# Kernel optimization log

Hardware: AMD Instinct MI355X
Metric: run time of the kernel (lower is better)

## Reference

```python
import jax, jax.numpy as jnp
import numpy as np

N_NODES = 100000
N_EDGES = 1600000
IN_DIM = 128
HID_DIM = 128
OUT_DIM = 16
N_GRAPHS = 128


def setup_inputs() -> dict:
    key = jax.random.key(0)
    ks = jax.random.split(key, 8)
    x = jax.random.normal(ks[0], (N_NODES, IN_DIM), dtype=jnp.float32)
    edge_index = jax.random.randint(ks[1], (2, N_EDGES), 0, N_NODES, dtype=jnp.int64)
    batch = jnp.sort(jax.random.randint(ks[2], (N_NODES,), 0, N_GRAPHS, dtype=jnp.int64))
    # GCNConv params (glorot-ish scale) and Linear params
    w1 = jax.random.normal(ks[3], (IN_DIM, HID_DIM), dtype=jnp.float32) / np.sqrt(IN_DIM)
    b1 = jnp.zeros((HID_DIM,), dtype=jnp.float32)
    w2 = jax.random.normal(ks[4], (HID_DIM, HID_DIM), dtype=jnp.float32) / np.sqrt(HID_DIM)
    b2 = jnp.zeros((HID_DIM,), dtype=jnp.float32)
    wc = jax.random.normal(ks[5], (HID_DIM, OUT_DIM), dtype=jnp.float32) / np.sqrt(HID_DIM)
    bc = jnp.zeros((OUT_DIM,), dtype=jnp.float32)
    return {"x": x, "edge_index": edge_index, "batch": batch,
            "w1": w1, "b1": b1, "w2": w2, "b2": b2, "wc": wc, "bc": bc}


def _gcn_layer(h, src, dst, w, b, n_nodes):
    # h: [N, Fin]; src/dst: [E+N] (self-loops already appended)
    h = h @ w  # [N, Fout]
    ones = jnp.ones_like(dst, dtype=h.dtype)
    deg = jax.ops.segment_sum(ones, dst, num_segments=n_nodes)  # [N]
    dinv = jnp.where(deg > 0, jax.lax.rsqrt(deg), 0.0)
    norm = dinv[src] * dinv[dst]  # [E+N]
    msg = h[src] * norm[:, None]  # gather + scale, [E+N, Fout]
    out = jax.ops.segment_sum(msg, dst, num_segments=n_nodes)  # scatter-add
    return out + b


def reference(x, edge_index, batch, w1, b1, w2, b2, wc, bc):
    n = x.shape[0]
    loop = jnp.arange(n, dtype=edge_index.dtype)
    src = jnp.concatenate([edge_index[0], loop])  # add self-loops (PyG default)
    dst = jnp.concatenate([edge_index[1], loop])

    h = jax.nn.relu(_gcn_layer(x, src, dst, w1, b1, n))
    h = jax.nn.relu(_gcn_layer(h, src, dst, w2, b2, n))

    # global mean pool over graphs
    sums = jax.ops.segment_sum(h, batch, num_segments=N_GRAPHS)  # [G, H]
    cnt = jax.ops.segment_sum(jnp.ones((n,), h.dtype), batch, num_segments=N_GRAPHS)
    pooled = sums / jnp.maximum(cnt, 1.0)[:, None]

    return pooled @ wc + bc  # [G, OUT_DIM]
```

## Files before the change

### kernel.cpp

```cpp
#include <hip/hip_runtime.h>
#include <hip/hip_bf16.h>
#include <stdint.h>

#define NN 100000
#define NE 1600000
#define FDIM 128
#define NGRAPH 128
#define ODIM 16
#define NBKT 391
#define CAP 4608
#define PCAP 8704
#define SCHUNK 4096
#define NSCAT ((NE + SCHUNK - 1) / SCHUNK)
#define NSTARTB ((NN + 255) / 256)

typedef __attribute__((ext_vector_type(8))) short short8;
typedef __attribute__((ext_vector_type(8))) unsigned short ushort8;
typedef __attribute__((ext_vector_type(4))) float f32x4;
typedef __attribute__((ext_vector_type(2))) float f32x2;
typedef __attribute__((ext_vector_type(4))) int i32x4;

__device__ __forceinline__ float blo(unsigned int p) { return __uint_as_float(p << 16); }
__device__ __forceinline__ float bhi(unsigned int p) { return __uint_as_float(p & 0xffff0000u); }
__device__ __forceinline__ unsigned short f2b(float f) {
    unsigned int u = __float_as_uint(f);
    unsigned int r = (u + 0x7fffu + ((u >> 16) & 1u)) >> 16;
    return (unsigned short)r;
}
__device__ __forceinline__ unsigned int cvt2(float lo, float hi) {
    __hip_bfloat162 b = __float22bfloat162_rn(float2{lo, hi});
    return *reinterpret_cast<unsigned int*>(&b);
}

__device__ __forceinline__ int detect_w(const int* __restrict__ ei) {
    int lane = threadIdx.x & 63;
    int v = ei[2 * lane + 1];
    return (__ballot(v != 0) == 0ULL) ? 1 : 0;
}
__device__ __forceinline__ int ld_idx(const int* __restrict__ p, long long i, int w) {
    return w ? p[2 * i] : p[i];
}

__global__ void __launch_bounds__(256) k_prep(
    const float* __restrict__ w1, const float* __restrict__ w2,
    unsigned short* __restrict__ wt1, unsigned short* __restrict__ wt2,
    const int* __restrict__ ei, const int* __restrict__ batch,
    int* __restrict__ gstart, int* __restrict__ bcursor,
    unsigned short* __restrict__ xws)
{
    int b = blockIdx.x, t = threadIdx.x;
    if (b < 128) {
        int idx = b * 256 + t;
        int which = idx >> 14, r = idx & 16383;
        int k = r >> 7, j = r & 127;
        const float* w = which ? w2 : w1;
        unsigned short* wt = which ? wt2 : wt1;
        wt[j * 128 + k] = f2b(w[k * 128 + j]);
    } else if (b < 128 + NSTARTB) {
        int w = detect_w(ei);
        int i = (b - 128) * 256 + t;
        if (i < NN) {
            int bb = ld_idx(batch, i, w);
            int prev = (i == 0) ? -1 : ld_idx(batch, i - 1, w);
            for (int g = prev + 1; g <= bb; ++g) gstart[g] = i;
            if (i == NN - 1)
                for (int g = bb + 1; g <= NGRAPH; ++g) gstart[g] = NN;
        }
    } else {
        int i = (b - 128 - NSTARTB) * 256 + t;
        if (i < NBKT) bcursor[i] = i * CAP;
        if (b == 128 + NSTARTB && t < FDIM) xws[(size_t)NN * FDIM + t] = 0;
    }
}

__global__ void __launch_bounds__(512) k_scat(const int* __restrict__ ei,
                                              int* __restrict__ bcursor,
                                              unsigned int* __restrict__ rec) {
    __shared__ int hist[NBKT];
    __shared__ int gbase[NBKT];
    __shared__ int lcur[NBKT];
    int t = threadIdx.x;
    int w = detect_w(ei);
    for (int i = t; i < NBKT; i += 512) hist[i] = 0;
    __syncthreads();
    long long e0 = (long long)blockIdx.x * SCHUNK;
    unsigned int myrec[8];
    int mybkt[8];
    #pragma unroll
    for (int j = 0; j < 8; ++j) {
        long long e = e0 + j * 512 + t;
        if (e < NE) {
            int s = ld_idx(ei, e, w);
            int d = ld_idx(ei, NE + e, w);
            mybkt[j] = d >> 8;
            myrec[j] = (unsigned int)s | ((unsigned int)(d & 255) << 17);
            atomicAdd(&hist[mybkt[j]], 1);
        } else mybkt[j] = -1;
    }
    __syncthreads();
    for (int i = t; i < NBKT; i += 512) {
        int c = hist[i];
        gbase[i] = c ? atomicAdd(&bcursor[i], c) : 0;
        lcur[i] = 0;
    }
    __syncthreads();
    #pragma unroll
    for (int j = 0; j < 8; ++j) {
        int b = mybkt[j];
        if (b >= 0) {
            int r = atomicAdd(&lcur[b], 1);
            int p = gbase[b] + r;
            if (p < (b + 1) * CAP) rec[p] = myrec[j];
        }
    }
}

__global__ void __launch_bounds__(256) k_bucket(const unsigned int* __restrict__ rec,
                                                const int* __restrict__ bcursor,
                                                int* __restrict__ csr,
                                                int2* __restrict__ odeg,
                                                float* __restrict__ dinv) {
    __shared__ unsigned int rbuf[CAP];
    __shared__ int srcout[PCAP];
    __shared__ int hist[256], scn[256], cur[256];
    int b = blockIdx.x, t = threadIdx.x;
    int rbase = b * CAP;
    int cnt = bcursor[b] - rbase;
    if (cnt > CAP) cnt = CAP;
    hist[t] = 0;
    __syncthreads();
    for (int j = t; j < cnt; j += 256) {
        unsigned int r = __builtin_nontemporal_load(&rec[rbase + j]);
        rbuf[j] = r;
        atomicAdd(&hist[r >> 17], 1);
    }
    for (int j = t; j < PCAP; j += 256) srcout[j] = NN << 8;
    __syncthreads();
    int node = (b << 8) + t;
    int v = hist[t];
    int pv = (node < NN) ? ((v + 16) & ~15) : 0;
    scn[t] = pv;
    __syncthreads();
    for (int o = 1; o < 256; o <<= 1) {
        int tv = (t >= o) ? scn[t - o] : 0;
        __syncthreads();
        scn[t] += tv;
        __syncthreads();
    }
    int pexcl = scn[t] - pv;
    cur[t] = pexcl;
    int obase = b * PCAP;
    if (node < NN) {
        odeg[node] = make_int2(obase + pexcl, pv);
        dinv[node] = rsqrtf((float)(v + 1));
        srcout[pexcl + v] = node << 8;
    }
    __syncthreads();
    for (int j = t; j < cnt; j += 256) {
        unsigned int r = rbuf[j];
        int p = atomicAdd(&cur[r >> 17], 1);
        srcout[p] = (int)(r & 0x1FFFFu) << 8;
    }
    __syncthreads();
    int total = scn[255];
    for (int j = t; j < total; j += 256) csr[obase + j] = srcout[j];
}

#define LWS 136
template <bool BF16IN>
__global__ void __launch_bounds__(256) k_gemm(
    const void* __restrict__ Xv,
    const unsigned short* __restrict__ WT,
    const float* __restrict__ dinv,
    unsigned short* __restrict__ OUT)
{
    __shared__ unsigned short lw[128 * LWS];
    int tid = threadIdx.x;
    for (int it = 0; it < 8; ++it) {
        int vidx = it * 256 + tid;
        int j = vidx >> 4, kc = vidx & 15;
        ushort8 v = *(const ushort8*)(WT + j * 128 + kc * 8);
        *(ushort8*)(&lw[j * LWS + kc * 8]) = v;
    }
    __syncthreads();

    int wave = tid >> 6, lane = tid & 63;
    int quad = lane >> 4, n16 = lane & 15;
    int row0 = (blockIdx.x * 4 + wave) * 16;
    if (row0 >= NN) return;

    f32x4 acc[8];
    for (int ct = 0; ct < 8; ++ct) acc[ct] = (f32x4){0.f, 0.f, 0.f, 0.f};

    const int arow = row0 + n16;
    for (int kk = 0; kk < 4; ++kk) {
        short8 a;
        if (BF16IN) {
            a = *(const short8*)((const unsigned short*)Xv + (size_t)arow * 128 + kk * 32 + quad * 8);
        } else {
            const float* ap = (const float*)Xv + (size_t)arow * 128 + kk * 32 + quad * 8;
            float4 a01 = *(const float4*)(ap);
            float4 a23 = *(const float4*)(ap + 4);
            uint4 P;
            P.x = cvt2(a01.x, a01.y);
            P.y = cvt2(a01.z, a01.w);
            P.z = cvt2(a23.x, a23.y);
            P.w = cvt2(a23.z, a23.w);
            a = *(short8*)&P;
        }
        for (int ct = 0; ct < 8; ++ct) {
            short8 b = *(const short8*)(&lw[(ct * 16 + n16) * LWS + kk * 32 + quad * 8]);
            acc[ct] = __builtin_amdgcn_mfma_f32_16x16x32_bf16(a, b, acc[ct], 0, 0, 0);
        }
    }
    for (int r = 0; r < 4; ++r) {
        int row = row0 + quad * 4 + r;
        float dv = dinv[row];
        for (int ct = 0; ct < 8; ++ct)
            OUT[(size_t)row * 128 + ct * 16 + n16] = f2b(acc[ct][r] * dv);
    }
}

__device__ __forceinline__ void acc8(f32x2* a2, uint4 q) {
    a2[0] += (f32x2){blo(q.x), bhi(q.x)};
    a2[1] += (f32x2){blo(q.y), bhi(q.y)};
    a2[2] += (f32x2){blo(q.z), bhi(q.z)};
    a2[3] += (f32x2){blo(q.w), bhi(q.w)};
}

__global__ void __launch_bounds__(256) k_agg(
    const unsigned short* __restrict__ XWS,
    const int* __restrict__ csr,
    const int2* __restrict__ odeg,
    const float* __restrict__ dinv,
    const float* __restrict__ bias,
    unsigned short* __restrict__ H)
{
    int wave = threadIdx.x >> 6, lane = threadIdx.x & 63;
    int v = blockIdx.x * 4 + wave;
    int g = lane >> 4, f = lane & 15;
    int2 od = odeg[v];
    int beg = od.x, pdeg = od.y;
    const char* xb = (const char*)XWS;
    unsigned fo = (unsigned)(f * 16);
    const int* cp = csr + beg + 4 * g;

    f32x2 a2[4];
    a2[0] = (f32x2){0.f, 0.f}; a2[1] = (f32x2){0.f, 0.f};
    a2[2] = (f32x2){0.f, 0.f}; a2[3] = (f32x2){0.f, 0.f};

    int j = 0;
    int pd2 = pdeg & ~31;
    for (; j < pd2; j += 32) {
        i32x4 ca = __builtin_nontemporal_load((const i32x4*)(cp + j));
        i32x4 cb = __builtin_nontemporal_load((const i32x4*)(cp + j + 16));
        uint4 q0 = *(const uint4*)(xb + ((unsigned)ca.x + fo));
        uint4 q1 = *(const uint4*)(xb + ((unsigned)ca.y + fo));
        uint4 q2 = *(const uint4*)(xb + ((unsigned)ca.z + fo));
        uint4 q3 = *(const uint4*)(xb + ((unsigned)ca.w + fo));
        uint4 q4 = *(const uint4*)(xb + ((unsigned)cb.x + fo));
        uint4 q5 = *(const uint4*)(xb + ((unsigned)cb.y + fo));
        uint4 q6 = *(const uint4*)(xb + ((unsigned)cb.z + fo));
        uint4 q7 = *(const uint4*)(xb + ((unsigned)cb.w + fo));
        acc8(a2, q0); acc8(a2, q1); acc8(a2, q2); acc8(a2, q3);
        acc8(a2, q4); acc8(a2, q5); acc8(a2, q6); acc8(a2, q7);
    }
    if (j < pdeg) {
        i32x4 ca = __builtin_nontemporal_load((const i32x4*)(cp + j));
        uint4 q0 = *(const uint4*)(xb + ((unsigned)ca.x + fo));
        uint4 q1 = *(const uint4*)(xb + ((unsigned)ca.y + fo));
        uint4 q2 = *(const uint4*)(xb + ((unsigned)ca.z + fo));
        uint4 q3 = *(const uint4*)(xb + ((unsigned)ca.w + fo));
        acc8(a2, q0); acc8(a2, q1); acc8(a2, q2); acc8(a2, q3);
    }
    #pragma unroll
    for (int i = 0; i < 4; ++i) {
        a2[i].x += __shfl_xor(a2[i].x, 16);
        a2[i].y += __shfl_xor(a2[i].y, 16);
        a2[i].x += __shfl_xor(a2[i].x, 32);
        a2[i].y += __shfl_xor(a2[i].y, 32);
    }
    if (g == 0) {
        float dv = dinv[v];
        float4 b0 = *(const float4*)(bias + f * 8);
        float4 b1 = *(const float4*)(bias + f * 8 + 4);
        uint4 o;
        o.x = cvt2(fmaxf(fmaf(a2[0].x, dv, b0.x), 0.f), fmaxf(fmaf(a2[0].y, dv, b0.y), 0.f));
        o.y = cvt2(fmaxf(fmaf(a2[1].x, dv, b0.z), 0.f), fmaxf(fmaf(a2[1].y, dv, b0.w), 0.f));
        o.z = cvt2(fmaxf(fmaf(a2[2].x, dv, b1.x), 0.f), fmaxf(fmaf(a2[2].y, dv, b1.y), 0.f));
        o.w = cvt2(fmaxf(fmaf(a2[3].x, dv, b1.z), 0.f), fmaxf(fmaf(a2[3].y, dv, b1.w), 0.f));
        *(uint4*)(H + (size_t)v * FDIM + f * 8) = o;
    }
}

__global__ void __launch_bounds__(512) k_poolcls(
    const unsigned short* __restrict__ H, const int* __restrict__ gstart,
    const float* __restrict__ wc, const float* __restrict__ bc,
    float* __restrict__ out)
{
    __shared__ float red[1024];
    __shared__ float pl[FDIM];
    int g = blockIdx.x;
    int t = threadIdx.x;
    int pair = t & 63;
    int seg = t >> 6;
    int beg = gstart[g], end = gstart[g + 1];
    float a0 = 0.f, a1 = 0.f;
    for (int i = beg + seg; i < end; i += 8) {
        unsigned int q = *(const unsigned int*)(H + (size_t)i * FDIM + 2 * pair);
        a0 += blo(q); a1 += bhi(q);
    }
    red[t] = a0; red[512 + t] = a1;
    __syncthreads();
    if (seg == 0) {
        float s0 = 0.f, s1 = 0.f;
        #pragma unroll
        for (int k = 0; k < 8; ++k) {
            s0 += red[pair + 64 * k];
            s1 += red[512 + pair + 64 * k];
        }
        float inv = 1.f / fmaxf((float)(end - beg), 1.f);
        pl[2 * pair] = s0 * inv;
        pl[2 * pair + 1] = s1 * inv;
    }
    __syncthreads();
    if (t < 256) {
        int o = t & 15, fs = t >> 4;
        float acc = 0.f;
        #pragma unroll
        for (int k = 0; k < 8; ++k)
            acc += pl[fs * 8 + k] * wc[(fs * 8 + k) * ODIM + o];
        red[t] = acc;
    }
    __syncthreads();
    if (t < 16) {
        float s = bc[t];
        #pragma unroll
        for (int k = 0; k < 16; ++k) s += red[k * 16 + t];
        out[g * ODIM + t] = s;
    }
}

extern "C" void kernel_launch(void* const* d_in, const int* in_sizes, int n_in,
                              void* d_out, int out_size, void* d_ws, size_t ws_size,
                              hipStream_t stream) {
    const float* x   = (const float*)d_in[0];
    const int* ei    = (const int*)d_in[1];
    const int* batch = (const int*)d_in[2];
    const float* w1  = (const float*)d_in[3];
    const float* b1  = (const float*)d_in[4];
    const float* w2  = (const float*)d_in[5];
    const float* b2  = (const float*)d_in[6];
    const float* wc  = (const float*)d_in[7];
    const float* bc  = (const float*)d_in[8];
    float* out = (float*)d_out;

    char* ws = (char*)d_ws;
    size_t off = 0;
    auto alloc = [&](size_t bytes) -> void* {
        off = (off + 255) & ~(size_t)255;
        void* p = ws + off;
        off += bytes;
        return p;
    };
    int*   bcursor = (int*)alloc(NBKT * 4);
    int2*  odeg    = (int2*)alloc((size_t)NN * 8);
    float* dinv    = (float*)alloc(NN * 4);
    int*   gstart  = (int*)alloc((NGRAPH + 1) * 4);
    unsigned int* rec = (unsigned int*)alloc((size_t)NBKT * CAP * 4);
    int*   csr     = (int*)alloc((size_t)NBKT * PCAP * 4 + 256);
    unsigned short* wt1 = (unsigned short*)alloc(128 * 128 * 2);
    unsigned short* wt2 = (unsigned short*)alloc(128 * 128 * 2);
    unsigned short* xws = (unsigned short*)alloc((size_t)(NN + 1) * FDIM * 2);
    unsigned short* h   = (unsigned short*)alloc((size_t)NN * FDIM * 2);

    k_prep<<<128 + NSTARTB + 2, 256, 0, stream>>>(w1, w2, wt1, wt2, ei, batch, gstart, bcursor, xws);
    k_scat<<<NSCAT, 512, 0, stream>>>(ei, bcursor, rec);
    k_bucket<<<NBKT, 256, 0, stream>>>(rec, bcursor, csr, odeg, dinv);

    k_gemm<false><<<(NN / 16 + 3) / 4, 256, 0, stream>>>(x, wt1, dinv, xws);
    k_agg<<<NN / 4, 256, 0, stream>>>(xws, csr, odeg, dinv, b1, h);
    k_gemm<true><<<(NN / 16 + 3) / 4, 256, 0, stream>>>(h, wt2, dinv, xws);
    k_agg<<<NN / 4, 256, 0, stream>>>(xws, csr, odeg, dinv, b2, h);
    k_poolcls<<<NGRAPH, 512, 0, stream>>>(h, gstart, wc, bc, out);
}
```

Before: 312.8 us.

## Slice feature matrices into 16-column planes for cache-local gather aggregation

Stores the intermediate node-feature matrices as eight 16-feature slices (32 bytes per node per slice) instead of row-major 128-wide rows. Aggregation blocks are now assigned one slice each, and each node is handled by two lanes that read the CSR indices serially. Because a slice covers about 3.2 MB, the random gathers should stay within L2 rather than spanning the full 25 MB feature matrix. The cost is that CSR indices are re-read eight times, per-lane index loads are scalar and serial, and load balance across high-degree nodes gets worse.

```diff
diff --git a/kernel.cpp b/kernel.cpp
--- a/kernel.cpp
+++ b/kernel.cpp
@@ -13,12 +13,13 @@
 #define SCHUNK 4096
 #define NSCAT ((NE + SCHUNK - 1) / SCHUNK)
 #define NSTARTB ((NN + 255) / 256)
+#define SSTR ((NN + 1) * 16)
+#define NAGGB ((((NN) + 127) / 128) * 8)
 
 typedef __attribute__((ext_vector_type(8))) short short8;
 typedef __attribute__((ext_vector_type(8))) unsigned short ushort8;
 typedef __attribute__((ext_vector_type(4))) float f32x4;
 typedef __attribute__((ext_vector_type(2))) float f32x2;
-typedef __attribute__((ext_vector_type(4))) int i32x4;
 
 __device__ __forceinline__ float blo(unsigned int p) { return __uint_as_float(p << 16); }
 __device__ __forceinline__ float bhi(unsigned int p) { return __uint_as_float(p & 0xffff0000u); }
@@ -69,7 +70,10 @@
     } else {
         int i = (b - 128 - NSTARTB) * 256 + t;
         if (i < NBKT) bcursor[i] = i * CAP;
-        if (b == 128 + NSTARTB && t < FDIM) xws[(size_t)NN * FDIM + t] = 0;
+        if (b == 128 + NSTARTB && t < 128) {
+            int sl = t >> 4;
+            xws[(size_t)sl * SSTR + (size_t)NN * 16 + (t & 15)] = 0;
+        }
     }
 }
 
@@ -134,7 +138,7 @@
         rbuf[j] = r;
         atomicAdd(&hist[r >> 17], 1);
     }
-    for (int j = t; j < PCAP; j += 256) srcout[j] = NN << 8;
+    for (int j = t; j < PCAP; j += 256) srcout[j] = NN << 5;
     __syncthreads();
     int node = (b << 8) + t;
     int v = hist[t];
@@ -151,15 +155,15 @@
     cur[t] = pexcl;
     int obase = b * PCAP;
     if (node < NN) {
-        odeg[node] = make_int2(obase + pexcl, pv);
+        odeg[node] = make_int2(obase + pexcl, v + 1);
         dinv[node] = rsqrtf((float)(v + 1));
-        srcout[pexcl + v] = node << 8;
+        srcout[pexcl + v] = node << 5;
     }
     __syncthreads();
     for (int j = t; j < cnt; j += 256) {
         unsigned int r = rbuf[j];
         int p = atomicAdd(&cur[r >> 17], 1);
-        srcout[p] = (int)(r & 0x1FFFFu) << 8;
+        srcout[p] = (int)(r & 0x1FFFFu) << 5;
     }
     __syncthreads();
     int total = scn[255];
@@ -196,7 +200,9 @@
     for (int kk = 0; kk < 4; ++kk) {
         short8 a;
         if (BF16IN) {
-            a = *(const short8*)((const unsigned short*)Xv + (size_t)arow * 128 + kk * 32 + quad * 8);
+            const unsigned short* Hs = (const unsigned short*)Xv;
+            int sl = 2 * kk + (quad >> 1);
+            a = *(const short8*)(Hs + (size_t)sl * SSTR + (size_t)arow * 16 + (quad & 1) * 8);
         } else {
             const float* ap = (const float*)Xv + (size_t)arow * 128 + kk * 32 + quad * 8;
             float4 a01 = *(const float4*)(ap);
@@ -217,7 +223,7 @@
         int row = row0 + quad * 4 + r;
         float dv = dinv[row];
         for (int ct = 0; ct < 8; ++ct)
-            OUT[(size_t)row * 128 + ct * 16 + n16] = f2b(acc[ct][r] * dv);
+            OUT[(size_t)ct * SSTR + (size_t)row * 16 + n16] = f2b(acc[ct][r] * dv);
     }
 }
 
@@ -236,60 +242,46 @@
     const float* __restrict__ bias,
     unsigned short* __restrict__ H)
 {
+    int s = blockIdx.x & 7;
+    int grp = blockIdx.x >> 3;
     int wave = threadIdx.x >> 6, lane = threadIdx.x & 63;
-    int v = blockIdx.x * 4 + wave;
-    int g = lane >> 4, f = lane & 15;
-    int2 od = odeg[v];
-    int beg = od.x, pdeg = od.y;
-    const char* xb = (const char*)XWS;
-    unsigned fo = (unsigned)(f * 16);
-    const int* cp = csr + beg + 4 * g;
+    int p = lane >> 1, h = lane & 1;
+    int v = grp * 128 + wave * 32 + p;
+    bool act = v < NN;
+    int2 od = act ? odeg[v] : make_int2(0, 0);
+    int beg = od.x, n = od.y;
+    const char* xb = (const char*)XWS + (size_t)s * (SSTR * 2);
+    unsigned ho = (unsigned)(h * 16);
+    const int* cp = csr + beg;
 
     f32x2 a2[4];
     a2[0] = (f32x2){0.f, 0.f}; a2[1] = (f32x2){0.f, 0.f};
     a2[2] = (f32x2){0.f, 0.f}; a2[3] = (f32x2){0.f, 0.f};
 
     int j = 0;
-    int pd2 = pdeg & ~31;
-    for (; j < pd2; j += 32) {
-        i32x4 ca = __builtin_nontemporal_load((const i32x4*)(cp + j));
-        i32x4 cb = __builtin_nontemporal_load((const i32x4*)(cp + j + 16));
-        uint4 q0 = *(const uint4*)(xb + ((unsigned)ca.x + fo));
-        uint4 q1 = *(const uint4*)(xb + ((unsigned)ca.y + fo));
-        uint4 q2 = *(const uint4*)(xb + ((unsigned)ca.z + fo));
-        uint4 q3 = *(const uint4*)(xb + ((unsigned)ca.w + fo));
-        uint4 q4 = *(const uint4*)(xb + ((unsigned)cb.x + fo));
-        uint4 q5 = *(const uint4*)(xb + ((unsigned)cb.y + fo));
-        uint4 q6 = *(const uint4*)(xb + ((unsigned)cb.z + fo));
-        uint4 q7 = *(const uint4*)(xb + ((unsigned)cb.w + fo));
-        acc8(a2, q0); acc8(a2, q1); acc8(a2, q2); acc8(a2, q3);
-        acc8(a2, q4); acc8(a2, q5); acc8(a2, q6); acc8(a2, q7);
-    }
-    if (j < pdeg) {
-        i32x4 ca = __builtin_nontemporal_load((const i32x4*)(cp + j));
-        uint4 q0 = *(const uint4*)(xb + ((unsigned)ca.x + fo));
-        uint4 q1 = *(const uint4*)(xb + ((unsigned)ca.y + fo));
-        uint4 q2 = *(const uint4*)(xb + ((unsigned)ca.z + fo));
-        uint4 q3 = *(const uint4*)(xb + ((unsigned)ca.w + fo));
-        acc8(a2, q0); acc8(a2, q1); acc8(a2, q2); acc8(a2, q3);
-    }
-    #pragma unroll
-    for (int i = 0; i < 4; ++i) {
-        a2[i].x += __shfl_xor(a2[i].x, 16);
-        a2[i].y += __shfl_xor(a2[i].y, 16);
-        a2[i].x += __shfl_xor(a2[i].x, 32);
-        a2[i].y += __shfl_xor(a2[i].y, 32);
-    }
-    if (g == 0) {
+    for (; j + 2 <= n; j += 2) {
+        int c0 = cp[j], c1 = cp[j + 1];
+        uint4 q0 = *(const uint4*)(xb + ((unsigned)c0 + ho));
+        uint4 q1 = *(const uint4*)(xb + ((unsigned)c1 + ho));
+        acc8(a2, q0);
+        acc8(a2, q1);
+    }
+    if (j < n) {
+        int c0 = cp[j];
+        uint4 q0 = *(const uint4*)(xb + ((unsigned)c0 + ho));
+        acc8(a2, q0);
+    }
+    if (act) {
         float dv = dinv[v];
-        float4 b0 = *(const float4*)(bias + f * 8);
-        float4 b1 = *(const float4*)(bias + f * 8 + 4);
+        const float* bp = bias + s * 16 + h * 8;
+        float4 b0 = *(const float4*)bp;
+        float4 b1 = *(const float4*)(bp + 4);
         uint4 o;
         o.x = cvt2(fmaxf(fmaf(a2[0].x, dv, b0.x), 0.f), fmaxf(fmaf(a2[0].y, dv, b0.y), 0.f));
         o.y = cvt2(fmaxf(fmaf(a2[1].x, dv, b0.z), 0.f), fmaxf(fmaf(a2[1].y, dv, b0.w), 0.f));
         o.z = cvt2(fmaxf(fmaf(a2[2].x, dv, b1.x), 0.f), fmaxf(fmaf(a2[2].y, dv, b1.y), 0.f));
         o.w = cvt2(fmaxf(fmaf(a2[3].x, dv, b1.z), 0.f), fmaxf(fmaf(a2[3].y, dv, b1.w), 0.f));
-        *(uint4*)(H + (size_t)v * FDIM + f * 8) = o;
+        *(uint4*)((char*)H + (size_t)s * (SSTR * 2) + (size_t)v * 32 + ho) = o;
     }
 }
 
@@ -305,9 +297,11 @@
     int pair = t & 63;
     int seg = t >> 6;
     int beg = gstart[g], end = gstart[g + 1];
+    int f0 = 2 * pair;
+    const unsigned short* hp = H + (size_t)(f0 >> 4) * SSTR + (f0 & 15);
     float a0 = 0.f, a1 = 0.f;
     for (int i = beg + seg; i < end; i += 8) {
-        unsigned int q = *(const unsigned int*)(H + (size_t)i * FDIM + 2 * pair);
+        unsigned int q = *(const unsigned int*)(hp + (size_t)i * 16);
         a0 += blo(q); a1 += bhi(q);
     }
     red[t] = a0; red[512 + t] = a1;
@@ -371,16 +365,16 @@
     int*   csr     = (int*)alloc((size_t)NBKT * PCAP * 4 + 256);
     unsigned short* wt1 = (unsigned short*)alloc(128 * 128 * 2);
     unsigned short* wt2 = (unsigned short*)alloc(128 * 128 * 2);
-    unsigned short* xws = (unsigned short*)alloc((size_t)(NN + 1) * FDIM * 2);
-    unsigned short* h   = (unsigned short*)alloc((size_t)NN * FDIM * 2);
+    unsigned short* xws = (unsigned short*)alloc((size_t)8 * SSTR * 2);
+    unsigned short* h   = (unsigned short*)alloc((size_t)8 * SSTR * 2);
 
     k_prep<<<128 + NSTARTB + 2, 256, 0, stream>>>(w1, w2, wt1, wt2, ei, batch, gstart, bcursor, xws);
     k_scat<<<NSCAT, 512, 0, stream>>>(ei, bcursor, rec);
     k_bucket<<<NBKT, 256, 0, stream>>>(rec, bcursor, csr, odeg, dinv);
 
     k_gemm<false><<<(NN / 16 + 3) / 4, 256, 0, stream>>>(x, wt1, dinv, xws);
-    k_agg<<<NN / 4, 256, 0, stream>>>(xws, csr, odeg, dinv, b1, h);
+    k_agg<<<NAGGB, 256, 0, stream>>>(xws, csr, odeg, dinv, b1, h);
     k_gemm<true><<<(NN / 16 + 3) / 4, 256, 0, stream>>>(h, wt2, dinv, xws);
-    k_agg<<<NN / 4, 256, 0, stream>>>(xws, csr, odeg, dinv, b2, h);
+    k_agg<<<NAGGB, 256, 0, stream>>>(xws, csr, odeg, dinv, b2, h);
     k_poolcls<<<NGRAPH, 512, 0, stream>>>(h, gstart, wc, bc, out);
 }
```

Result: slower. 452.0 us (+44.5%).
